# Optimization experiments

Hardware: AMD Instinct MI355X
Metric: run time of the kernel (lower is better)

Reference implementation:

```python
import jax, jax.numpy as jnp
import numpy as np

EPS = 1e-5
HEADS, DK, DV = 8, 32, 64  # active_num_heads, active_key_dim, key_dim*attn_ratio


def _bn(x, g, b, m, v):
    # eval-mode BatchNorm2d over channel axis 1
    s = g * jax.lax.rsqrt(v + EPS)
    return x * s[None, :, None, None] + (b - m * s)[None, :, None, None]


def _bn_params(key, n):
    k1, k2, k3, k4 = jax.random.split(key, 4)
    gamma = 1.0 + 0.1 * jax.random.normal(k1, (n,), jnp.float32)
    beta = 0.1 * jax.random.normal(k2, (n,), jnp.float32)
    mean = 0.1 * jax.random.normal(k3, (n,), jnp.float32)
    var = jax.random.uniform(k4, (n,), jnp.float32, 0.5, 1.5)
    return gamma, beta, mean, var


def setup_inputs() -> dict:
    key = jax.random.key(0)
    ks = jax.random.split(key, 9)
    B, C, H, W = 8, 384, 32, 32
    Cqk, Cv = DK * HEADS, DV * HEADS  # 256, 512
    x = jax.random.normal(ks[0], (B, C, H, W), jnp.float32)
    w_q = jax.random.normal(ks[1], (Cqk, C), jnp.float32) / np.sqrt(C)
    w_k = jax.random.normal(ks[2], (Cqk, C), jnp.float32) / np.sqrt(C)
    w_v = jax.random.normal(ks[3], (Cv, C), jnp.float32) / np.sqrt(C)
    w_proj = jax.random.normal(ks[4], (C, Cv), jnp.float32) / np.sqrt(Cv)
    g_q, b_q, m_q, var_q = _bn_params(ks[5], Cqk)
    g_k, b_k, m_k, var_k = _bn_params(ks[6], Cqk)
    g_v, b_v, m_v, var_v = _bn_params(ks[7], Cv)
    g_p, b_p, m_p, var_p = _bn_params(ks[8], C)
    return dict(x=x, w_q=w_q, g_q=g_q, b_q=b_q, m_q=m_q, var_q=var_q,
                w_k=w_k, g_k=g_k, b_k=b_k, m_k=m_k, var_k=var_k,
                w_v=w_v, g_v=g_v, b_v=b_v, m_v=m_v, var_v=var_v,
                w_proj=w_proj, g_p=g_p, b_p=b_p, m_p=m_p, var_p=var_p)


def reference(x, w_q, g_q, b_q, m_q, var_q,
              w_k, g_k, b_k, m_k, var_k,
              w_v, g_v, b_v, m_v, var_v,
              w_proj, g_p, b_p, m_p, var_p):
    B, C, H, W = x.shape
    N = H * W
    # active config == max config, so dynamic index gathers are identity
    q = _bn(jnp.einsum('oc,bchw->bohw', w_q, x), g_q, b_q, m_q, var_q)
    k = _bn(jnp.einsum('oc,bchw->bohw', w_k, x), g_k, b_k, m_k, var_k)
    v = _bn(jnp.einsum('oc,bchw->bohw', w_v, x), g_v, b_v, m_v, var_v)
    q = q.reshape(B, HEADS, DK, N).transpose(0, 1, 3, 2)   # b h n d
    k = k.reshape(B, HEADS, DK, N)                          # b h d m
    v = v.reshape(B, HEADS, DV, N).transpose(0, 1, 3, 2)   # b h m e
    # NOTE: original forward does NOT apply self.scale
    attn = jax.nn.softmax(jnp.einsum('bhnd,bhdm->bhnm', q, k), axis=-1)
    out = jnp.einsum('bhnm,bhme->bhne', attn, v)
    out = out.transpose(0, 1, 3, 2).reshape(B, HEADS * DV, H, W)
    out = jax.nn.relu(out)
    out = _bn(jnp.einsum('oc,bchw->bohw', w_proj, out), g_p, b_p, m_p, var_p)
    return out
```

## Files before the change

### kernel.cpp

```cpp
#include <hip/hip_runtime.h>
#include <hip/hip_bf16.h>

#define DEVI __device__ __forceinline__

typedef __attribute__((ext_vector_type(8))) short s16x8;
typedef __attribute__((ext_vector_type(4))) short s16x4;
typedef __attribute__((ext_vector_type(4))) float f32x4;

#define LOG2E 1.4426950408889634f

DEVI short f2bs(float f) {
    unsigned u = __builtin_bit_cast(unsigned, f);
    unsigned r = (u + 0x7fffu + ((u >> 16) & 1u)) >> 16;
    return (short)r;
}

DEVI f32x4 mfma16(s16x8 a, s16x8 b, f32x4 c) {
    return __builtin_amdgcn_mfma_f32_16x16x32_bf16(a, b, c, 0, 0, 0);
}

DEVI void gl_lds16(const short* g, short* l) {
    __builtin_amdgcn_global_load_lds(
        (const __attribute__((address_space(1))) unsigned*)(const void*)g,
        (__attribute__((address_space(3))) unsigned*)(void*)l, 16, 0, 0);
}

__global__ __launch_bounds__(256) void k_prep(
    const float* __restrict__ x, short* __restrict__ xt,
    const float* __restrict__ wq, const float* __restrict__ wk,
    const float* __restrict__ wv, const float* __restrict__ wp,
    short* __restrict__ wqkv, short* __restrict__ wpb,
    const float* gq, const float* bq, const float* mq, const float* vq,
    const float* gk, const float* bk, const float* mk, const float* vk,
    const float* gv, const float* bv, const float* mv, const float* vv,
    const float* gp, const float* bp, const float* mp, const float* vp,
    float* s_qkv, float* t_qkv, float* s_p, float* t_p) {
    __shared__ float tile[32][33];
    const int bid = blockIdx.x;
    const int t = threadIdx.x;
    if (bid < 3072) {
        const int ct = bid % 12, nt = (bid / 12) % 32, b = bid / 384;
        {
            const int j = t & 31, i0 = (t >> 5) * 4;
            const float* src = x + ((size_t)b * 384 + (size_t)ct * 32) * 1024 + nt * 32;
#pragma unroll
            for (int ii = 0; ii < 4; ++ii)
                tile[i0 + ii][j] = src[(size_t)(i0 + ii) * 1024 + j];
        }
        __syncthreads();
        {
            const int ii = t & 31, j0 = (t >> 5) * 4;
            short* dst = xt + ((size_t)b * 1024 + (size_t)nt * 32) * 384 + ct * 32;
#pragma unroll
            for (int jj = 0; jj < 4; ++jj)
                dst[(size_t)(j0 + jj) * 384 + ii] = f2bs(tile[ii][j0 + jj]);
        }
        return;
    }
    int i = (bid - 3072) * 256 + t;
    if (i < 1024) {
        const float *g, *bb, *mm, *vv_;
        int o = i;
        float post = 1.0f;
        if (i < 256)      { g = gq; bb = bq; mm = mq; vv_ = vq; post = LOG2E; }
        else if (i < 512) { g = gk; bb = bk; mm = mk; vv_ = vk; o = i - 256; }
        else              { g = gv; bb = bv; mm = mv; vv_ = vv; o = i - 512; }
        float s = g[o] * rsqrtf(vv_[o] + 1e-5f);
        s_qkv[i] = s * post;
        t_qkv[i] = (bb[o] - mm[o] * s) * post;
        if (i < 384) {
            float sp = gp[i] * rsqrtf(vp[i] + 1e-5f);
            s_p[i] = sp;
            t_p[i] = bp[i] - mp[i] * sp;
        }
    }
    const int NQKV = 1024 * 384;
    if (i < NQKV) {
        int o = i / 384;
        float v;
        if (o < 256)      v = wq[i];
        else if (o < 512) v = wk[i - 256 * 384];
        else              v = wv[i - 512 * 384];
        wqkv[i] = f2bs(v);
    } else {
        int j = i - NQKV;
        if (j < 384 * 512) wpb[j] = f2bs(wp[j]);
    }
}

__global__ __launch_bounds__(256, 2) void k_gemm_qkv(
    const short* __restrict__ wqkv, const short* __restrict__ xt,
    const float* __restrict__ s_qkv, const float* __restrict__ t_qkv,
    short* __restrict__ Qw, short* __restrict__ Kw, short* __restrict__ Vw) {
    __shared__ short AB[2][16384];
    const int t = threadIdx.x, lane = t & 63, w = t >> 6;
    const int g = lane >> 4, l15 = lane & 15;
    const int wr = w >> 1, wc = w & 1;
    const int jb = blockIdx.x, mb = blockIdx.y;

    const int ar = t >> 3, au = t & 7;
    const int aperm = 8 * (au ^ (ar & 7));
    const short* gA = wqkv + (size_t)(mb * 128 + ar) * 384 + aperm;
    const short* gB = xt + (size_t)((size_t)jb * 128 + ar) * 384 + aperm;

    f32x4 acc[4][4];
#pragma unroll
    for (int mi = 0; mi < 4; ++mi)
#pragma unroll
        for (int ni = 0; ni < 4; ++ni) acc[mi][ni] = f32x4{0.f, 0.f, 0.f, 0.f};

    auto stage = [&](int kt, int buf) {
        short* base = AB[buf];
#pragma unroll
        for (int jj = 0; jj < 4; ++jj) {
            gl_lds16(gA + (size_t)(32 * jj) * 384 + kt * 64, base + t * 8 + jj * 2048);
            gl_lds16(gB + (size_t)(32 * jj) * 384 + kt * 64, base + 8192 + t * 8 + jj * 2048);
        }
    };

    stage(0, 0);
    __syncthreads();

    for (int kt = 0; kt < 6; ++kt) {
        if (kt < 5) stage(kt + 1, (kt + 1) & 1);
        const short* base = AB[kt & 1];
#pragma unroll
        for (int ksub = 0; ksub < 2; ++ksub) {
            const int kc = 8 * ((4 * ksub + g) ^ (l15 & 7));
            s16x8 a[4], b[4];
#pragma unroll
            for (int mi = 0; mi < 4; ++mi)
                a[mi] = *(const s16x8*)(base + (64 * wr + 16 * mi + l15) * 64 + kc);
#pragma unroll
            for (int ni = 0; ni < 4; ++ni)
                b[ni] = *(const s16x8*)(base + 8192 + (64 * wc + 16 * ni + l15) * 64 + kc);
#pragma unroll
            for (int mi = 0; mi < 4; ++mi)
#pragma unroll
                for (int ni = 0; ni < 4; ++ni)
                    acc[mi][ni] = mfma16(a[mi], b[ni], acc[mi][ni]);
        }
        __syncthreads();
    }

    const int m_base = mb * 128 + 64 * wr;
    const int j_base = jb * 128 + 64 * wc;
#pragma unroll
    for (int mi = 0; mi < 4; ++mi) {
        const int o0 = m_base + 16 * mi;
#pragma unroll
        for (int ni = 0; ni < 4; ++ni) {
            const int j = j_base + 16 * ni + l15;
            const int bb = j >> 10, n = j & 1023;
            if (o0 < 512) {
                const int o = o0 + 4 * g;
                const int isK = o0 >= 256;
                const int o2 = o - (isK ? 256 : 0);
                const int h = o2 >> 5, d0 = o2 & 31;
                s16x4 ov;
#pragma unroll
                for (int r = 0; r < 4; ++r)
                    ov[r] = f2bs(acc[mi][ni][r] * s_qkv[o + r] + t_qkv[o + r]);
                short* dst = (isK ? Kw : Qw) + (((size_t)bb * 8 + h) * 1024 + n) * 32 + d0;
                *(s16x4*)dst = ov;
            } else {
#pragma unroll
                for (int r = 0; r < 4; ++r) {
                    const int o = o0 + 4 * g + r;
                    float val = acc[mi][ni][r] * s_qkv[o] + t_qkv[o];
                    const int o2 = o - 512;
                    const int h = o2 >> 6, e = o2 & 63;
                    Vw[(((size_t)bb * 8 + h) * 64 + e) * 1024 + n] = f2bs(val);
                }
            }
        }
    }
}

__global__ __launch_bounds__(256, 2) void k_attn(const short* __restrict__ Qw,
                                                 const short* __restrict__ Kw,
                                                 const short* __restrict__ Vw,
                                                 short* __restrict__ Ow) {
    __shared__ short KV[2][12288];
    const int t = threadIdx.x, lane = t & 63, w = t >> 6;
    const int g = lane >> 4, l15 = lane & 15;
    const int low3 = blockIdx.x & 7;
    const int mid = blockIdx.x >> 3;
    const int rb = mid & 7;
    const int bh = ((mid >> 3) << 3) | low3;
    const int n_base = rb * 128 + w * 32;
    const short* Qb = Qw + (size_t)bh * (1024 * 32);
    const short* Kb = Kw + (size_t)bh * (1024 * 32);
    const short* Vb = Vw + (size_t)bh * (64 * 1024);

    s16x8 qf[2];
#pragma unroll
    for (int i = 0; i < 2; ++i)
        qf[i] = *(const s16x8*)(Qb + (size_t)(n_base + 16 * i + l15) * 32 + 8 * g);

    const s16x8 onesf = {0x3F80, 0x3F80, 0x3F80, 0x3F80, 0x3F80, 0x3F80, 0x3F80, 0x3F80};

    const int skr = t >> 2, sku = t & 3;
    const short* gK = Kb + (size_t)skr * 32 + 8 * (sku ^ (skr & 3));
    const int vr = t >> 4, vu = t & 15;
    const short* gV = Vb + (size_t)vr * 1024 + 8 * (vu ^ (vr & 7));

    f32x4 oacc[2][4], lacc[2];
#pragma unroll
    for (int niq = 0; niq < 2; ++niq) {
        lacc[niq] = f32x4{0.f, 0.f, 0.f, 0.f};
#pragma unroll
        for (int ei = 0; ei < 4; ++ei) oacc[niq][ei] = f32x4{0.f, 0.f, 0.f, 0.f};
    }

    const int krow = 8 * (l15 >> 2) + (l15 & 3);
    const int kcol = 8 * (g ^ (l15 & 3));

    auto stage = [&](int m0, int buf) {
        short* base = KV[buf];
        gl_lds16(gK + m0 * 32, base + t * 8);
        gl_lds16(gK + (m0 + 64) * 32, base + (t + 256) * 8);
#pragma unroll
        for (int jj = 0; jj < 4; ++jj)
            gl_lds16(gV + (size_t)(16 * jj) * 1024 + m0, base + 4096 + t * 8 + jj * 2048);
    };

    stage(0, 0);
    __syncthreads();

    for (int mt = 0; mt < 8; ++mt) {
        if (mt < 7) stage((mt + 1) * 128, (mt + 1) & 1);
        const short* base = KV[mt & 1];
#pragma unroll
        for (int msub = 0; msub < 2; ++msub) {
            const int mofs = 64 * msub;
            s16x8 kf[4];
            kf[0] = *(const s16x8*)(base + (krow + mofs + 0) * 32 + kcol);
            kf[1] = *(const s16x8*)(base + (krow + mofs + 4) * 32 + kcol);
            kf[2] = *(const s16x8*)(base + (krow + mofs + 32) * 32 + kcol);
            kf[3] = *(const s16x8*)(base + (krow + mofs + 36) * 32 + kcol);
            s16x8 vb[2][4];
#pragma unroll
            for (int ki = 0; ki < 2; ++ki)
#pragma unroll
                for (int ei = 0; ei < 4; ++ei) {
                    const int row = 16 * ei + l15;
                    vb[ki][ei] = *(const s16x8*)(base + 4096 + row * 128 +
                                                 8 * ((8 * msub + 4 * ki + g) ^ (row & 7)));
                }
            __builtin_amdgcn_s_setprio(1);
            f32x4 st[4][2];
#pragma unroll
            for (int mik = 0; mik < 4; ++mik)
#pragma unroll
                for (int niq = 0; niq < 2; ++niq)
                    st[mik][niq] = mfma16(kf[mik], qf[niq], f32x4{0.f, 0.f, 0.f, 0.f});
            __builtin_amdgcn_s_setprio(0);
            s16x4 pk[4][2];
#pragma unroll
            for (int mik = 0; mik < 4; ++mik)
#pragma unroll
                for (int niq = 0; niq < 2; ++niq) {
#pragma unroll
                    for (int r = 0; r < 4; ++r) {
                        float p = __builtin_amdgcn_exp2f(st[mik][niq][r]);
                        pk[mik][niq][r] =
                            __builtin_bit_cast(short, __float2bfloat16(p));
                    }
                }
            __builtin_amdgcn_s_setprio(1);
#pragma unroll
            for (int ki = 0; ki < 2; ++ki)
#pragma unroll
                for (int niq = 0; niq < 2; ++niq) {
                    s16x8 pb = __builtin_shufflevector(pk[2 * ki][niq], pk[2 * ki + 1][niq],
                                                       0, 1, 2, 3, 4, 5, 6, 7);
                    lacc[niq] = mfma16(onesf, pb, lacc[niq]);
#pragma unroll
                    for (int ei = 0; ei < 4; ++ei)
                        oacc[niq][ei] = mfma16(vb[ki][ei], pb, oacc[niq][ei]);
                }
            __builtin_amdgcn_s_setprio(0);
        }
        __syncthreads();
    }

    float li[2];
#pragma unroll
    for (int niq = 0; niq < 2; ++niq) li[niq] = __builtin_amdgcn_rcpf(lacc[niq][0]);

    const int b = bh >> 3, h = bh & 7;
#pragma unroll
    for (int niq = 0; niq < 2; ++niq) {
        const int n = n_base + 16 * niq + l15;
#pragma unroll
        for (int ei = 0; ei < 4; ++ei) {
            s16x4 ov;
#pragma unroll
            for (int r = 0; r < 4; ++r)
                ov[r] = f2bs(fmaxf(oacc[niq][ei][r] * li[niq], 0.f));
            *(s16x4*)(Ow + ((size_t)b * 1024 + n) * 512 + h * 64 + 16 * ei + 4 * g) = ov;
        }
    }
}

__global__ __launch_bounds__(256, 3) void k_proj(const short* __restrict__ wpb,
                                                 const short* __restrict__ Ow,
                                                 const float* __restrict__ s_p,
                                                 const float* __restrict__ t_p,
                                                 float* __restrict__ out) {
    __shared__ short AB[2][8192];
    const int t = threadIdx.x, lane = t & 63, w = t >> 6;
    const int g = lane >> 4, l15 = lane & 15;
    const int wr = w >> 1, wc = w & 1;
    const int jb = blockIdx.x, mb = blockIdx.y;

    const int ar = t >> 3, au = t & 7;
    const int aperm = 8 * (au ^ (ar & 7));
    const short* gA = wpb + (size_t)(mb * 64 + ar) * 512 + aperm;
    const short* gB = Ow + (size_t)((size_t)jb * 64 + ar) * 512 + aperm;

    f32x4 acc[2][2];
#pragma unroll
    for (int mi = 0; mi < 2; ++mi)
#pragma unroll
        for (int ni = 0; ni < 2; ++ni) acc[mi][ni] = f32x4{0.f, 0.f, 0.f, 0.f};

    auto stage = [&](int kt, int buf) {
        short* base = AB[buf];
#pragma unroll
        for (int jj = 0; jj < 2; ++jj) {
            gl_lds16(gA + (size_t)(32 * jj) * 512 + kt * 64, base + t * 8 + jj * 2048);
            gl_lds16(gB + (size_t)(32 * jj) * 512 + kt * 64, base + 4096 + t * 8 + jj * 2048);
        }
    };

    stage(0, 0);
    __syncthreads();

    for (int kt = 0; kt < 8; ++kt) {
        if (kt < 7) stage(kt + 1, (kt + 1) & 1);
        const short* base = AB[kt & 1];
#pragma unroll
        for (int ksub = 0; ksub < 2; ++ksub) {
            const int kc = 8 * ((4 * ksub + g) ^ (l15 & 7));
            s16x8 a[2], b[2];
#pragma unroll
            for (int mi = 0; mi < 2; ++mi)
                a[mi] = *(const s16x8*)(base + (32 * wr + 16 * mi + l15) * 64 + kc);
#pragma unroll
            for (int ni = 0; ni < 2; ++ni)
                b[ni] = *(const s16x8*)(base + 4096 + (32 * wc + 16 * ni + l15) * 64 + kc);
#pragma unroll
            for (int mi = 0; mi < 2; ++mi)
#pragma unroll
                for (int ni = 0; ni < 2; ++ni)
                    acc[mi][ni] = mfma16(a[mi], b[ni], acc[mi][ni]);
        }
        __syncthreads();
    }

    const int m_base = mb * 64 + 32 * wr;
    const int j_base = jb * 64 + 32 * wc;
#pragma unroll
    for (int mi = 0; mi < 2; ++mi) {
#pragma unroll
        for (int ni = 0; ni < 2; ++ni) {
            const int j = j_base + 16 * ni + l15;
            const int bb = j >> 10, n = j & 1023;
#pragma unroll
            for (int r = 0; r < 4; ++r) {
                const int c = m_base + 16 * mi + 4 * g + r;
                float v = acc[mi][ni][r] * s_p[c] + t_p[c];
                out[((size_t)bb * 384 + c) * 1024 + n] = v;
            }
        }
    }
}

extern "C" void kernel_launch(void* const* d_in, const int* in_sizes, int n_in,
                              void* d_out, int out_size, void* d_ws, size_t ws_size,
                              hipStream_t stream) {
    const float* x  = (const float*)d_in[0];
    const float* wq = (const float*)d_in[1];
    const float* gq = (const float*)d_in[2];
    const float* bq = (const float*)d_in[3];
    const float* mq = (const float*)d_in[4];
    const float* vq = (const float*)d_in[5];
    const float* wk = (const float*)d_in[6];
    const float* gk = (const float*)d_in[7];
    const float* bk = (const float*)d_in[8];
    const float* mk = (const float*)d_in[9];
    const float* vk = (const float*)d_in[10];
    const float* wv = (const float*)d_in[11];
    const float* gv = (const float*)d_in[12];
    const float* bv = (const float*)d_in[13];
    const float* mv = (const float*)d_in[14];
    const float* vv = (const float*)d_in[15];
    const float* wp = (const float*)d_in[16];
    const float* gp = (const float*)d_in[17];
    const float* bp = (const float*)d_in[18];
    const float* mp = (const float*)d_in[19];
    const float* vp = (const float*)d_in[20];
    float* out = (float*)d_out;

    char* ws = (char*)d_ws;
    size_t off = 0;
    auto alloc = [&](size_t bytes) {
        char* p = ws + off;
        off += (bytes + 255) & ~(size_t)255;
        return p;
    };
    short* xt    = (short*)alloc((size_t)8 * 1024 * 384 * 2);
    short* wqkv  = (short*)alloc((size_t)1024 * 384 * 2);
    short* wpb   = (short*)alloc((size_t)384 * 512 * 2);
    float* s_qkv = (float*)alloc(1024 * 4);
    float* t_qkv = (float*)alloc(1024 * 4);
    float* s_p   = (float*)alloc(384 * 4);
    float* t_p   = (float*)alloc(384 * 4);
    short* Qw    = (short*)alloc((size_t)8 * 8 * 1024 * 32 * 2);
    short* Kw    = (short*)alloc((size_t)8 * 8 * 1024 * 32 * 2);
    short* Vw    = (short*)alloc((size_t)8 * 8 * 64 * 1024 * 2);
    short* Ow    = (short*)alloc((size_t)8 * 1024 * 512 * 2);
    (void)ws_size; (void)in_sizes; (void)n_in; (void)out_size;

    k_prep<<<dim3(3072 + 2304), 256, 0, stream>>>(
        x, xt, wq, wk, wv, wp, wqkv, wpb,
        gq, bq, mq, vq, gk, bk, mk, vk, gv, bv, mv, vv, gp, bp, mp, vp,
        s_qkv, t_qkv, s_p, t_p);
    k_gemm_qkv<<<dim3(64, 8), 256, 0, stream>>>(wqkv, xt, s_qkv, t_qkv, Qw, Kw, Vw);
    k_attn<<<dim3(512), 256, 0, stream>>>(Qw, Kw, Vw, Ow);
    k_proj<<<dim3(128, 6), 256, 0, stream>>>(wpb, Ow, s_p, t_p, out);
}
```

Measured before the change: 48.98 us.

## Triple-buffer LDS staging in attention and projection kernels with partial vmcnt waits

Both the attention and projection kernels move from a double-buffered to a triple-buffered LDS pipeline that prefetches two tiles ahead. Full __syncthreads waits are replaced by s_waitcnt vmcnt(N) plus s_barrier, so loads for the newer tile can stay in flight while the current one is consumed. This aims to hide global-to-LDS latency better. In exchange it uses more shared memory (72KB per block in attention), which could reduce occupancy, and it depends on hand-counted outstanding-load numbers being right.

```diff
diff --git a/kernel.cpp b/kernel.cpp
--- a/kernel.cpp
+++ b/kernel.cpp
@@ -181,7 +181,7 @@
                                                  const short* __restrict__ Kw,
                                                  const short* __restrict__ Vw,
                                                  short* __restrict__ Ow) {
-    __shared__ short KV[2][12288];
+    __shared__ short KV[3][12288];
     const int t = threadIdx.x, lane = t & 63, w = t >> 6;
     const int g = lane >> 4, l15 = lane & 15;
     const int low3 = blockIdx.x & 7;
@@ -226,11 +226,13 @@
     };
 
     stage(0, 0);
-    __syncthreads();
+    stage(128, 1);
+    asm volatile("s_waitcnt vmcnt(6)" ::: "memory");
+    __builtin_amdgcn_s_barrier();
 
     for (int mt = 0; mt < 8; ++mt) {
-        if (mt < 7) stage((mt + 1) * 128, (mt + 1) & 1);
-        const short* base = KV[mt & 1];
+        if (mt < 6) stage((mt + 2) * 128, (mt + 2) % 3);
+        const short* base = KV[mt % 3];
 #pragma unroll
         for (int msub = 0; msub < 2; ++msub) {
             const int mofs = 64 * msub;
@@ -282,7 +284,14 @@
                 }
             __builtin_amdgcn_s_setprio(0);
         }
-        __syncthreads();
+        if (mt < 7) {
+            if (mt < 6) {
+                asm volatile("s_waitcnt vmcnt(6)" ::: "memory");
+            } else {
+                asm volatile("s_waitcnt vmcnt(0)" ::: "memory");
+            }
+            __builtin_amdgcn_s_barrier();
+        }
     }
 
     float li[2];
@@ -309,7 +318,7 @@
                                                  const float* __restrict__ s_p,
                                                  const float* __restrict__ t_p,
                                                  float* __restrict__ out) {
-    __shared__ short AB[2][8192];
+    __shared__ short AB[3][8192];
     const int t = threadIdx.x, lane = t & 63, w = t >> 6;
     const int g = lane >> 4, l15 = lane & 15;
     const int wr = w >> 1, wc = w & 1;
@@ -336,11 +345,13 @@
     };
 
     stage(0, 0);
-    __syncthreads();
+    stage(1, 1);
+    asm volatile("s_waitcnt vmcnt(4)" ::: "memory");
+    __builtin_amdgcn_s_barrier();
 
     for (int kt = 0; kt < 8; ++kt) {
-        if (kt < 7) stage(kt + 1, (kt + 1) & 1);
-        const short* base = AB[kt & 1];
+        if (kt < 6) stage(kt + 2, (kt + 2) % 3);
+        const short* base = AB[kt % 3];
 #pragma unroll
         for (int ksub = 0; ksub < 2; ++ksub) {
             const int kc = 8 * ((4 * ksub + g) ^ (l15 & 7));
@@ -357,7 +368,14 @@
                 for (int ni = 0; ni < 2; ++ni)
                     acc[mi][ni] = mfma16(a[mi], b[ni], acc[mi][ni]);
         }
-        __syncthreads();
+        if (kt < 7) {
+            if (kt < 6) {
+                asm volatile("s_waitcnt vmcnt(4)" ::: "memory");
+            } else {
+                asm volatile("s_waitcnt vmcnt(0)" ::: "memory");
+            }
+            __builtin_amdgcn_s_barrier();
+        }
     }
 
     const int m_base = mb * 64 + 32 * wr;
```

New measurement: 49.31 us. Within noise of the previous version (+0.7%).
